# Optimization experiments

Hardware: AMD Instinct MI355X
Metric: run time of the kernel (lower is better)

## Reference

```python
import jax, jax.numpy as jnp
import numpy as np

N, M, DIST, HEADS, D, C, DFFN = 16384, 16, 2, 8, 256, 64, 512
DH = D // HEADS
GRID = 128
BLOCK = 2048  # mirrors torch batch_size loop in find_neighboring_voxels_optimized
EPS = 1e-5


def _neighbors(coords_f, src, m, dist):
    """Blockwise Manhattan-distance topk neighbor gather.
    coords_f: (N,3) float voxel coords; src: (N,D) features.
    Returns (N, m, D) neighbor features, zero-filled where fewer than m in range."""
    n = coords_f.shape[0]
    qblocks = coords_f.reshape(-1, BLOCK, 3)

    def one_block(cb):
        # (BLOCK, N) Manhattan distances
        d = jnp.abs(cb[:, None, :] - coords_f[None, :, :]).sum(-1)
        d = jnp.where(d <= dist, d, jnp.inf)
        vals, idx = jax.lax.top_k(-d, m)          # nearest m (self first: dist 0)
        valid = (vals > -jnp.inf)[..., None]
        return jnp.where(valid, src[idx], jnp.zeros((), src.dtype))

    return jax.lax.map(one_block, qblocks).reshape(n, m, src.shape[-1])


def _layernorm(x, g, b):
    mu = x.mean(-1, keepdims=True)
    var = ((x - mu) ** 2).mean(-1, keepdims=True)
    return (x - mu) * jax.lax.rsqrt(var + EPS) * g + b


def setup_inputs() -> dict:
    key = jax.random.key(0)
    ks = jax.random.split(key, 32)
    p = lambda i, shape, s: jax.random.normal(ks[i], shape, dtype=jnp.float32) * s
    z = lambda shape: jnp.zeros(shape, dtype=jnp.float32)
    o = lambda shape: jnp.ones(shape, dtype=jnp.float32)
    return {
        "coords": jax.random.randint(ks[0], (N, 3), 0, GRID, dtype=jnp.int32),
        "features": jax.random.normal(ks[1], (N, C), dtype=jnp.float32),
        "pe_w1": p(2, (3, D // 2), 0.5), "pe_b1": z((D // 2,)),
        "pe_w2": p(3, (D // 2, D), 0.08), "pe_b2": z((D,)),
        "proj_w": p(4, (C, D), 0.12), "proj_b": z((D,)),
        "wq": p(5, (D, D), 0.06), "bq": z((D,)),
        "wk": p(6, (D, D), 0.06), "bk": z((D,)),
        "wv": p(7, (D, D), 0.06), "bv": z((D,)),
        "wo": p(8, (D, D), 0.06), "bo": z((D,)),
        "ffn_w1": p(9, (D, DFFN), 0.06), "ffn_b1": z((DFFN,)),
        "ffn_w2": p(10, (DFFN, D), 0.04), "ffn_b2": z((D,)),
        "ln_g": o((D,)), "ln_b": z((D,)),
        "fus_w1": p(11, (D, C), 0.06), "fus_b1": z((C,)),
        "fus_w2": p(12, (2 * C, C), 0.09), "fus_b2": z((C,)),
        "bn_g": o((C,)), "bn_b": z((C,)),
    }


def reference(coords, features, pe_w1, pe_b1, pe_w2, pe_b2, proj_w, proj_b,
              wq, bq, wk, bk, wv, bv, wo, bo,
              ffn_w1, ffn_b1, ffn_w2, ffn_b2, ln_g, ln_b,
              fus_w1, fus_b1, fus_w2, fus_b2, bn_g, bn_b):
    coords_f = coords.astype(jnp.float32)
    # dynamic learnable positional encoding on normalized coords
    xn = coords_f / (GRID - 1)
    pe = jax.nn.relu(xn @ pe_w1 + pe_b1) @ pe_w2 + pe_b2
    src = features @ proj_w + proj_b + pe                       # (N, D)

    nf = _neighbors(coords_f, src, M, DIST)                     # (N, M, D)
    query = nf[:, 0, :]                                         # (N, D) self-feature

    # multihead attention: query len 1, key len M, batch N
    q = (query @ wq + bq).reshape(N, HEADS, DH)
    k = (nf @ wk + bk).reshape(N, M, HEADS, DH)
    v = (nf @ wv + bv).reshape(N, M, HEADS, DH)
    scores = jnp.einsum('nhd,nmhd->nhm', q, k) / jnp.sqrt(jnp.float32(DH))
    attn = jax.nn.softmax(scores, axis=-1)
    ao = jnp.einsum('nhm,nmhd->nhd', attn, v).reshape(N, D) @ wo + bo  # (N, D)

    # FFN with residual + LayerNorm (dropout=0 / eval)
    h = jax.nn.relu(ao @ ffn_w1 + ffn_b1) @ ffn_w2 + ffn_b2
    y = _layernorm(ao + h, ln_g, ln_b)                          # (N, D)

    # EnhancedFusion: project, concat, linear, BatchNorm1d (batch stats), ReLU
    t = y @ fus_w1 + fus_b1                                     # (N, C)
    f = jnp.concatenate([features, t], axis=1) @ fus_w2 + fus_b2
    mu = f.mean(0)
    var = ((f - mu) ** 2).mean(0)
    f = (f - mu) * jax.lax.rsqrt(var + EPS) * bn_g + bn_b
    return jax.nn.relu(f)                                       # (N, C)
```

## Files before the change

### kernel.cpp

```cpp
#include <hip/hip_runtime.h>
#include <stdint.h>

typedef unsigned short u16;
typedef unsigned int   u32;
typedef __attribute__((ext_vector_type(8))) short short8;
typedef __attribute__((ext_vector_type(4))) float f32x4;

static constexpr int kN = 16384;
static constexpr float kEPS = 1e-5f;

__device__ __forceinline__ u16 f2bf(float x) {
  u32 u = __float_as_uint(x);
  u32 r = (u + 0x7fffu + ((u >> 16) & 1u)) >> 16;
  return (u16)r;
}
__device__ __forceinline__ float bf2f(u16 x) {
  return __uint_as_float(((u32)x) << 16);
}
__device__ __forceinline__ void ldbf8(const u16* p, float* o) {
  uint4 v = *(const uint4*)p;
  o[0] = __uint_as_float(v.x << 16);  o[1] = __uint_as_float(v.x & 0xffff0000u);
  o[2] = __uint_as_float(v.y << 16);  o[3] = __uint_as_float(v.y & 0xffff0000u);
  o[4] = __uint_as_float(v.z << 16);  o[5] = __uint_as_float(v.z & 0xffff0000u);
  o[6] = __uint_as_float(v.w << 16);  o[7] = __uint_as_float(v.w & 0xffff0000u);
}
__device__ __forceinline__ void gll16(const u16* g, u16* l) {
  __builtin_amdgcn_global_load_lds(
      (const __attribute__((address_space(1))) void*)g,
      (__attribute__((address_space(3))) void*)l, 16, 0, 0);
}

struct WSet {
  const float* s[6]; u16* d[6];
  int K[6]; int N[6]; int dstride[6]; int coff[6];
};

__global__ __launch_bounds__(256) void k_setup(WSet ws,
                                               u32* __restrict__ zero_area,
                                               const float* __restrict__ proj_b,
                                               const float* __restrict__ pe_b2,
                                               const float* __restrict__ uw1,
                                               const float* __restrict__ ub1,
                                               const float* __restrict__ uw2,
                                               const float* __restrict__ ub2,
                                               u16* __restrict__ W2f,
                                               float* __restrict__ bbf,
                                               const int* __restrict__ coords,
                                               const float* __restrict__ feats,
                                               const float* __restrict__ pw1,
                                               const float* __restrict__ pb1,
                                               u16* __restrict__ A1,
                                               u16* __restrict__ A2,
                                               const float* __restrict__ wq,
                                               const float* __restrict__ wk,
                                               const float* __restrict__ wv,
                                               const float* __restrict__ proj_w_f,
                                               const float* __restrict__ pe_w2_f,
                                               u16* __restrict__ W1K,
                                               float* __restrict__ bcomb,
                                               const float* __restrict__ wo_f,
                                               const float* __restrict__ fw1_f,
                                               const float* __restrict__ bo_f,
                                               const float* __restrict__ fb1_f,
                                               u16* __restrict__ woK,
                                               float* __restrict__ bcomb2) {
  int w = blockIdx.y;
  if (w == 6) {
    int idx = blockIdx.x * 256 + threadIdx.x;
    if (idx < 33088) zero_area[idx] = 0u;
    return;
  }
  if (w == 7) {
    int n = blockIdx.x;
    if (n >= 64) return;
    int k = threadIdx.x;
    float s = 0.f;
    for (int j = 0; j < 64; j++) s += uw1[k * 64 + j] * uw2[(64 + j) * 64 + n];
    W2f[n * 320 + k] = f2bf(s);
    if (k < 64) W2f[n * 320 + 256 + k] = f2bf(uw2[k * 64 + n]);
    if (k == 0) {
      float b = ub2[n];
      for (int j = 0; j < 64; j++) b += ub1[j] * uw2[(64 + j) * 64 + n];
      bbf[n] = b;
    }
    return;
  }
  if (w == 8) {
    int r0 = blockIdx.x * 32;
#pragma unroll
    for (int s = 0; s < 3; s++) {
      int j = threadIdx.x + s * 256;
      int row = j / 24, seg = j % 24;
      int n = r0 + row;
      u16 o[8];
      if (seg < 8) {
        const float* fp = feats + (size_t)n * 64 + seg * 8;
        float4 a = *(const float4*)fp;
        float4 b = *(const float4*)(fp + 4);
        o[0] = f2bf(a.x); o[1] = f2bf(a.y); o[2] = f2bf(a.z); o[3] = f2bf(a.w);
        o[4] = f2bf(b.x); o[5] = f2bf(b.y); o[6] = f2bf(b.z); o[7] = f2bf(b.w);
        *(uint4*)(A2 + (size_t)n * 320 + 256 + seg * 8) = *(uint4*)o;
      } else {
        int jj0 = (seg - 8) * 8;
        float x0 = (float)coords[n * 3 + 0] * (1.f / 127.f);
        float x1 = (float)coords[n * 3 + 1] * (1.f / 127.f);
        float x2 = (float)coords[n * 3 + 2] * (1.f / 127.f);
#pragma unroll
        for (int u = 0; u < 8; u++) {
          int jj = jj0 + u;
          float hv = pb1[jj] + x0 * pw1[jj] + x1 * pw1[128 + jj] + x2 * pw1[256 + jj];
          o[u] = f2bf(fmaxf(hv, 0.f));
        }
      }
      *(uint4*)(A1 + (size_t)n * 192 + seg * 8) = *(uint4*)o;
    }
    return;
  }
  if (w == 9) {
    int bx = blockIdx.x;
    if (bx < 3) {
      const float* wsel = (bx == 0) ? wq : (bx == 1) ? wk : wv;
      int c = threadIdx.x;
      float s = 0.f;
      for (int d = 0; d < 256; d++) s += (proj_b[d] + pe_b2[d]) * wsel[d * 256 + c];
      bcomb[bx * 256 + c] = s;
    } else if (bx < 27) {
      int i0 = (bx - 3) * 2048 + threadIdx.x * 8;
      const float* src = (i0 < 16384) ? (proj_w_f + i0) : (pe_w2_f + (i0 - 16384));
      float4 a = *(const float4*)src;
      float4 b = *(const float4*)(src + 4);
      u16 o[8];
      o[0] = f2bf(a.x); o[1] = f2bf(a.y); o[2] = f2bf(a.z); o[3] = f2bf(a.w);
      o[4] = f2bf(b.x); o[5] = f2bf(b.y); o[6] = f2bf(b.z); o[7] = f2bf(b.w);
      *(uint4*)(W1K + i0) = *(uint4*)o;
    } else if (bx < 59) {
      int i0 = (bx - 27) * 2048 + threadIdx.x * 8;
      float4 a = *(const float4*)(wo_f + i0);
      float4 b = *(const float4*)(wo_f + i0 + 4);
      u16 o[8];
      o[0] = f2bf(a.x); o[1] = f2bf(a.y); o[2] = f2bf(a.z); o[3] = f2bf(a.w);
      o[4] = f2bf(b.x); o[5] = f2bf(b.y); o[6] = f2bf(b.z); o[7] = f2bf(b.w);
      *(uint4*)(woK + i0) = *(uint4*)o;
    } else if (bx < 61) {
      int n2 = (bx - 59) * 256 + threadIdx.x;
      float s = fb1_f[n2];
      for (int d = 0; d < 256; d++) s += bo_f[d] * fw1_f[d * 512 + n2];
      bcomb2[n2] = s;
    }
    return;
  }
  const float* S = ws.s[w]; u16* D = ws.d[w];
  int K = ws.K[w], N = ws.N[w], ds = ws.dstride[w], co = ws.coff[w];
  int ntx = N >> 5, tiles = ntx * (K >> 5);
  int t = blockIdx.x;
  if (t >= tiles) return;
  int n0 = (t % ntx) * 32, k0 = (t / ntx) * 32;
  __shared__ float st[32][33];
  int tr = threadIdx.x >> 3, tc4 = (threadIdx.x & 7) * 4;
  float4 v = *(const float4*)(S + (size_t)(k0 + tr) * N + n0 + tc4);
  st[tc4 + 0][tr] = v.x; st[tc4 + 1][tr] = v.y;
  st[tc4 + 2][tr] = v.z; st[tc4 + 3][tr] = v.w;
  __syncthreads();
  u16 o4[4];
  o4[0] = f2bf(st[tr][tc4 + 0]); o4[1] = f2bf(st[tr][tc4 + 1]);
  o4[2] = f2bf(st[tr][tc4 + 2]); o4[3] = f2bf(st[tr][tc4 + 3]);
  *(uint2*)(D + (size_t)(n0 + tr) * ds + co + k0 + tc4) = *(uint2*)o4;
}

__global__ __launch_bounds__(256) void k_combo(const u16* __restrict__ qkvT,
                                               const u16* __restrict__ W1K,
                                               u16* __restrict__ Wcomb,
                                               const u16* __restrict__ fw1T,
                                               const u16* __restrict__ woK,
                                               u16* __restrict__ Wcomb2,
                                               const int* __restrict__ coords,
                                               u32* __restrict__ cnt) {
  int y = blockIdx.y;
  if (y >= 20) {
    int n = ((y - 20) * 4 + blockIdx.x) * 256 + threadIdx.x;
    int c = coords[n * 3] * 128 + coords[n * 3 + 1];
    atomicAdd(&cnt[c], 1u);
    return;
  }
  const u16 *A, *WT; u16* C; int K, N, bm, bn;
  if (y < 12) {
    if (blockIdx.x >= 3) return;
    A = qkvT; WT = W1K; C = Wcomb; K = 256; N = 192;
    bm = y * 64; bn = blockIdx.x * 64;
  } else {
    A = fw1T; WT = woK; C = Wcomb2; K = 256; N = 256;
    bm = (y - 12) * 64; bn = blockIdx.x * 64;
  }
  __shared__ __align__(16) char smem[16384];
  u16* AsB = (u16*)smem;
  u16* BsB = AsB + 2 * 64 * 32;
  u16* tile = (u16*)smem;
  const int tid = threadIdx.x;
  const int wave = tid >> 6, lane = tid & 63;
  const int wr = (wave >> 1) * 32, wc = (wave & 1) * 32;
  const int fr = lane & 15, fk = (lane >> 4) * 8, rq = (lane >> 4) * 4;
  const int grow = tid >> 2, gko = (tid & 3) * 8;

  f32x4 acc[2][2];
#pragma unroll
  for (int i = 0; i < 2; i++)
#pragma unroll
    for (int j = 0; j < 2; j++)
#pragma unroll
      for (int r = 0; r < 4; r++) acc[i][j][r] = 0.f;

  for (int k0 = 0; k0 < K; k0 += 64) {
#pragma unroll
    for (int h = 0; h < 2; h++) {
      gll16(A + (size_t)(bm + grow) * K + k0 + h * 32 + gko, AsB + h * 2048 + tid * 8);
      gll16(WT + (size_t)(bn + grow) * K + k0 + h * 32 + gko, BsB + h * 2048 + tid * 8);
    }
    __syncthreads();
#pragma unroll
    for (int h = 0; h < 2; h++) {
      short8 af[2], bg[2];
#pragma unroll
      for (int i = 0; i < 2; i++)
        af[i] = *(const short8*)&AsB[h * 2048 + (wr + i * 16 + fr) * 32 + fk];
#pragma unroll
      for (int j = 0; j < 2; j++)
        bg[j] = *(const short8*)&BsB[h * 2048 + (wc + j * 16 + fr) * 32 + fk];
#pragma unroll
      for (int i = 0; i < 2; i++)
#pragma unroll
        for (int j = 0; j < 2; j++)
          acc[i][j] = __builtin_amdgcn_mfma_f32_16x16x32_bf16(af[i], bg[j], acc[i][j], 0, 0, 0);
    }
    __syncthreads();
  }
#pragma unroll
  for (int j = 0; j < 2; j++) {
    int ccl = wc + j * 16 + fr;
#pragma unroll
    for (int i = 0; i < 2; i++) {
      int rl = wr + i * 16 + rq;
#pragma unroll
      for (int r = 0; r < 4; r++) tile[(rl + r) * 72 + ccl] = f2bf(acc[i][j][r]);
    }
  }
  __syncthreads();
#pragma unroll
  for (int t = 0; t < 2; t++) {
    int idx = t * 256 + tid;
    int row = idx >> 3, c8 = (idx & 7) * 8;
    *(uint4*)(C + (size_t)(bm + row) * N + bn + c8) = *(const uint4*)&tile[row * 72 + c8];
  }
}

__global__ __launch_bounds__(256) void k_scatter(const int* __restrict__ coords,
                                                 const u32* __restrict__ cnt,
                                                 u32* __restrict__ startb,
                                                 u32* __restrict__ cursor,
                                                 u32* __restrict__ pts) {
  __shared__ u32 sb[16384];
  __shared__ u32 wsum[4];
  int t = threadIdx.x;
  int lane = t & 63, wid = t >> 6;
  int base = t * 64;
  u32 s = 0;
  for (int i = 0; i < 64; i++) s += cnt[base + i];
  u32 v = s;
#pragma unroll
  for (int off = 1; off < 64; off <<= 1) {
    u32 u = __shfl_up(v, off);
    if (lane >= off) v += u;
  }
  if (lane == 63) wsum[wid] = v;
  __syncthreads();
  u32 woff = 0;
  for (int w2 = 0; w2 < wid; w2++) woff += wsum[w2];
  u32 run = woff + v - s;
  for (int i = 0; i < 64; i++) { sb[base + i] = run; run += cnt[base + i]; }
  __syncthreads();
  startb[blockIdx.x * 256 + t] = sb[blockIdx.x * 256 + t];
  int n = blockIdx.x * 256 + t;
  int x = coords[n * 3], y = coords[n * 3 + 1], z = coords[n * 3 + 2];
  int c = x * 128 + y;
  u32 slot = atomicAdd(&cursor[c], 1u);
  pts[sb[c] + slot] = ((u32)z << 14) | (u32)n;
}

template <int BM, int BN, int ACT, bool SEL>
__global__ __launch_bounds__(256) void k_mgemm(
    const u16* __restrict__ A, const u16* __restrict__ WT,
    const float* __restrict__ bias,
    u16* __restrict__ Cout,
    int M, int K, int N, int lda, int ldc,
    const int* __restrict__ coords,
    const u32* __restrict__ startb,
    const u32* __restrict__ cnt,
    const u32* __restrict__ pts,
    int* __restrict__ idxo) {
  if (SEL && (int)blockIdx.y >= M / BM) {
    int sb = ((int)blockIdx.y - M / BM) * gridDim.x + blockIdx.x;
    if (sb >= 64) return;
    int gid = sb * 256 + threadIdx.x;
    u32 pk = pts[gid];
    int n = (int)(pk & 16383u);
    int z = (int)(pk >> 14);
    int x = coords[n * 3], y = coords[n * 3 + 1];
    u32 best[16];
#pragma unroll
    for (int j = 0; j < 16; j++) best[j] = 0xFFFFFFFFu;
    const int dxs[13] = {0, -1, 1, 0, 0, -2, 2, 0, 0, -1, -1, 1, 1};
    const int dys[13] = {0, 0, 0, -1, 1, 0, 0, -2, 2, -1, 1, -1, 1};
    const int dbs[13] = {0, 1, 1, 1, 1, 2, 2, 2, 2, 2, 2, 2, 2};
#pragma unroll
    for (int t = 0; t < 13; t++) {
      int xx = x + dxs[t], yy = y + dys[t];
      if (xx < 0 || xx > 127 || yy < 0 || yy > 127) continue;
      int c = xx * 128 + yy;
      u32 s0 = startb[c], e0 = s0 + cnt[c];
      for (u32 i = s0; i < e0; ++i) {
        u32 p = pts[i];
        int zq = (int)(p >> 14);
        int id = (int)(p & 16383u);
        int az = z - zq; az = az < 0 ? -az : az;
        int dd = dbs[t] + az;
        u32 key = (dd <= 2) ? (((u32)dd << 14) | (u32)id) : 0xFFFFFFFFu;
#pragma unroll
        for (int j = 0; j < 16; j++) {
          u32 lo = min(best[j], key);
          u32 hi = max(best[j], key);
          best[j] = lo; key = hi;
        }
      }
    }
#pragma unroll
    for (int j = 0; j < 16; j++)
      idxo[gid * 16 + j] = (best[j] == 0xFFFFFFFFu) ? -1 : (int)(best[j] & 16383u);
    return;
  }

  constexpr int FM = BM / 32, FN = BN / 32;
  constexpr int RA = BM / 64, RB = BN / 64;
  constexpr int BNP = BN + 8;
  constexpr int STAGE = (BM + BN) * 128;
  constexpr int TILEB = BM * BNP * 2;
  constexpr int SMEMB = STAGE > TILEB ? STAGE : TILEB;
  __shared__ __align__(16) char smem[SMEMB];
  u16* AsB = (u16*)smem;
  u16* BsB = AsB + 2 * BM * 32;
  u16* tile = (u16*)smem;
  const int tid = threadIdx.x;
  const int wave = tid >> 6, lane = tid & 63;
  const int bm = blockIdx.y * BM, bn = blockIdx.x * BN;
  const int wr = (wave >> 1) * (BM / 2), wc = (wave & 1) * (BN / 2);
  const int fr = lane & 15, fk = (lane >> 4) * 8, rq = (lane >> 4) * 4;

  f32x4 acc[FM][FN];
#pragma unroll
  for (int i = 0; i < FM; i++)
#pragma unroll
    for (int j = 0; j < FN; j++)
#pragma unroll
      for (int r = 0; r < 4; r++) acc[i][j][r] = 0.f;

  for (int k0 = 0; k0 < K; k0 += 64) {
#pragma unroll
    for (int h = 0; h < 2; h++) {
#pragma unroll
      for (int r = 0; r < RA; r++) {
        int g2 = r * 256 + tid;
        gll16(A + (size_t)(bm + (g2 >> 2)) * lda + k0 + h * 32 + (g2 & 3) * 8,
              AsB + h * BM * 32 + g2 * 8);
      }
#pragma unroll
      for (int r = 0; r < RB; r++) {
        int g2 = r * 256 + tid;
        gll16(WT + (size_t)(bn + (g2 >> 2)) * K + k0 + h * 32 + (g2 & 3) * 8,
              BsB + h * BN * 32 + g2 * 8);
      }
    }
    __syncthreads();
#pragma unroll
    for (int h = 0; h < 2; h++) {
      short8 af[FM], bg[FN];
#pragma unroll
      for (int i = 0; i < FM; i++)
        af[i] = *(const short8*)&AsB[h * BM * 32 + (wr + i * 16 + fr) * 32 + fk];
#pragma unroll
      for (int j = 0; j < FN; j++)
        bg[j] = *(const short8*)&BsB[h * BN * 32 + (wc + j * 16 + fr) * 32 + fk];
#pragma unroll
      for (int i = 0; i < FM; i++)
#pragma unroll
        for (int j = 0; j < FN; j++)
          acc[i][j] = __builtin_amdgcn_mfma_f32_16x16x32_bf16(af[i], bg[j], acc[i][j], 0, 0, 0);
    }
    __syncthreads();
  }

#pragma unroll
  for (int j = 0; j < FN; j++) {
    int ccl = wc + j * 16 + fr;
    float bval = bias ? bias[bn + ccl] : 0.f;
#pragma unroll
    for (int i = 0; i < FM; i++) {
      int rl = wr + i * 16 + rq;
#pragma unroll
      for (int r = 0; r < 4; r++) {
        float v = acc[i][j][r] + bval;
        if (ACT) v = fmaxf(v, 0.f);
        tile[(rl + r) * BNP + ccl] = f2bf(v);
      }
    }
  }
  __syncthreads();
  constexpr int RPW = BN / 8;
  constexpr int PT = BM * BN / 8 / 256;
#pragma unroll
  for (int t = 0; t < PT; t++) {
    int idx = t * 256 + tid;
    int row = idx / RPW, c8 = (idx % RPW) * 8;
    *(uint4*)(Cout + (size_t)(bm + row) * ldc + bn + c8) =
        *(const uint4*)&tile[row * BNP + c8];
  }
}

__global__ __launch_bounds__(256) void k_attn(const u16* __restrict__ QKV,
                                              const u32* __restrict__ pts,
                                              const int* __restrict__ idx,
                                              const float* __restrict__ bq,
                                              const float* __restrict__ bk,
                                              const float* __restrict__ bv,
                                              u16* __restrict__ outp) {
  int gid = blockIdx.x * 256 + threadIdx.x;
  int s4 = gid >> 3;
  int n = (int)(pts[s4] & 16383u), h = gid & 7;
  const int* ip = idx + s4 * 16;
  const int hb = h * 32;
  float q[32];
  {
    int i0 = ip[0];
    const u16* qp = QKV + (size_t)i0 * 768 + hb;
#pragma unroll
    for (int j = 0; j < 32; j += 8) ldbf8(qp + j, &q[j]);
#pragma unroll
    for (int j = 0; j < 32; j++) q[j] += bq[hb + j];
  }
  float qbk = 0.f;
#pragma unroll
  for (int j = 0; j < 32; j++) qbk += q[j] * bk[hb + j];
  float s[16]; int ii[16];
#pragma unroll
  for (int m = 0; m < 16; m++) {
    int i = ip[m]; ii[m] = i;
    float d = qbk;
    if (i >= 0) {
      const u16* kp = QKV + (size_t)i * 768 + 256 + hb;
      float kv[32];
#pragma unroll
      for (int j = 0; j < 32; j += 8) ldbf8(kp + j, &kv[j]);
#pragma unroll
      for (int j = 0; j < 32; j++) d += q[j] * kv[j];
    }
    s[m] = d * 0.17677669529663689f;
  }
  float mx = s[0];
#pragma unroll
  for (int m = 1; m < 16; m++) mx = fmaxf(mx, s[m]);
  float sum = 0.f;
#pragma unroll
  for (int m = 0; m < 16; m++) { s[m] = __expf(s[m] - mx); sum += s[m]; }
  float inv = 1.f / sum;
  float o[32];
#pragma unroll
  for (int j = 0; j < 32; j++) o[j] = 0.f;
#pragma unroll
  for (int m = 0; m < 16; m++) {
    if (ii[m] >= 0) {
      const u16* vp = QKV + (size_t)ii[m] * 768 + 512 + hb;
      float vv[32];
#pragma unroll
      for (int j = 0; j < 32; j += 8) ldbf8(vp + j, &vv[j]);
#pragma unroll
      for (int j = 0; j < 32; j++) o[j] += s[m] * vv[j];
    }
  }
  u16* op = outp + (size_t)n * 768 + hb;
#pragma unroll
  for (int j = 0; j < 32; j += 8) {
    u16 tmp[8];
#pragma unroll
    for (int jj = 0; jj < 8; jj++) tmp[jj] = f2bf(o[j + jj] * inv + bv[hb + j + jj]);
    *(uint4*)(op + j) = *(uint4*)tmp;
  }
}

__global__ __launch_bounds__(256) void k_ffn2f(const u16* __restrict__ AH,
                                               const u16* __restrict__ WTBIG,
                                               const float* __restrict__ bo,
                                               const float* __restrict__ fb2,
                                               const float* __restrict__ g,
                                               const float* __restrict__ b,
                                               const u16* __restrict__ A2,
                                               const u16* __restrict__ W2f,
                                               const float* __restrict__ bbf,
                                               float* __restrict__ fB,
                                               float* __restrict__ pS,
                                               float* __restrict__ pQ) {
  constexpr int BM = 64, BN = 256, FM = 2, FN = 8;
  constexpr int ADP2 = 328;
  __shared__ __align__(16) char smem[BM * ADP2 * 2];
  __shared__ __align__(16) u16 Bs2[2][2048];
  __shared__ float lnS[64][2], lnQ[64][2];
  __shared__ float colS[64][2], colQ[64][2];
  u16* AsB = (u16*)smem;
  u16* BsB = AsB + 2 * BM * 32;
  u16* aT  = (u16*)smem;
  const int tid = threadIdx.x;
  const int wave = tid >> 6, lane = tid & 63;
  const int bm = blockIdx.x * BM;
  const int wr = (wave >> 1) * 32, wc = (wave & 1) * 128;
  const int fr = lane & 15, fk = (lane >> 4) * 8, rq = (lane >> 4) * 4;

  f32x4 acc[FM][FN];
#pragma unroll
  for (int i = 0; i < FM; i++)
#pragma unroll
    for (int j = 0; j < FN; j++)
#pragma unroll
      for (int r = 0; r < 4; r++) acc[i][j][r] = 0.f;

  for (int k0 = 0; k0 < 768; k0 += 64) {
#pragma unroll
    for (int h = 0; h < 2; h++) {
      {
        int g2 = tid;
        gll16(AH + (size_t)(bm + (g2 >> 2)) * 768 + k0 + h * 32 + (g2 & 3) * 8,
              AsB + h * BM * 32 + g2 * 8);
      }
#pragma unroll
      for (int r = 0; r < 4; r++) {
        int g2 = r * 256 + tid;
        gll16(WTBIG + (size_t)(g2 >> 2) * 768 + k0 + h * 32 + (g2 & 3) * 8,
              BsB + h * BN * 32 + g2 * 8);
      }
    }
    __syncthreads();
#pragma unroll
    for (int h = 0; h < 2; h++) {
      short8 af[FM], bg[FN];
#pragma unroll
      for (int i = 0; i < FM; i++)
        af[i] = *(const short8*)&AsB[h * BM * 32 + (wr + i * 16 + fr) * 32 + fk];
#pragma unroll
      for (int j = 0; j < FN; j++)
        bg[j] = *(const short8*)&BsB[h * BN * 32 + (wc + j * 16 + fr) * 32 + fk];
#pragma unroll
      for (int i = 0; i < FM; i++)
#pragma unroll
        for (int j = 0; j < FN; j++)
          acc[i][j] = __builtin_amdgcn_mfma_f32_16x16x32_bf16(af[i], bg[j], acc[i][j], 0, 0, 0);
    }
    __syncthreads();
  }

#pragma unroll
  for (int j = 0; j < FN; j++) {
    int cc = wc + j * 16 + fr;
    float bval = bo[cc] + fb2[cc];
#pragma unroll
    for (int i = 0; i < FM; i++)
#pragma unroll
      for (int r = 0; r < 4; r++) acc[i][j][r] += bval;
  }
#pragma unroll
  for (int i = 0; i < FM; i++) {
#pragma unroll
    for (int r = 0; r < 4; r++) {
      float sm = 0.f, sq = 0.f;
#pragma unroll
      for (int j = 0; j < FN; j++) { float t = acc[i][j][r]; sm += t; sq += t * t; }
#pragma unroll
      for (int off = 1; off < 16; off <<= 1) {
        sm += __shfl_xor(sm, off);
        sq += __shfl_xor(sq, off);
      }
      if (fr == 0) {
        int row = wr + i * 16 + rq + r;
        lnS[row][wave & 1] = sm;
        lnQ[row][wave & 1] = sq;
      }
    }
  }
  __syncthreads();
#pragma unroll
  for (int i = 0; i < FM; i++) {
#pragma unroll
    for (int r = 0; r < 4; r++) {
      int row = wr + i * 16 + rq + r;
      float sm = lnS[row][0] + lnS[row][1];
      float sq = lnQ[row][0] + lnQ[row][1];
      float mu = sm * (1.f / 256.f);
      float var = sq * (1.f / 256.f) - mu * mu;
      float rstd = rsqrtf(var + kEPS);
#pragma unroll
      for (int j = 0; j < FN; j++) {
        int cc = wc + j * 16 + fr;
        float val = (acc[i][j][r] - mu) * rstd * g[cc] + b[cc];
        aT[row * ADP2 + cc] = f2bf(val);
      }
    }
  }
#pragma unroll
  for (int t = 0; t < 2; t++) {
    int idx = t * 256 + tid;
    int row = idx >> 3, c8 = (idx & 7) * 8;
    *(uint4*)&aT[row * ADP2 + 256 + c8] =
        *(const uint4*)(A2 + (size_t)(bm + row) * 320 + 256 + c8);
  }
  __syncthreads();

  const int wr3 = (wave >> 1) * 32, wc3 = (wave & 1) * 32;
  const int grow = tid >> 2, gko = (tid & 3) * 8;
  f32x4 acc2[2][2];
#pragma unroll
  for (int i = 0; i < 2; i++)
#pragma unroll
    for (int j = 0; j < 2; j++)
#pragma unroll
      for (int r = 0; r < 4; r++) acc2[i][j][r] = 0.f;
  for (int k0 = 0; k0 < 320; k0 += 64) {
#pragma unroll
    for (int h = 0; h < 2; h++)
      gll16(W2f + (size_t)grow * 320 + k0 + h * 32 + gko, Bs2[h] + tid * 8);
    __syncthreads();
#pragma unroll
    for (int h = 0; h < 2; h++) {
      short8 af[2], bg[2];
#pragma unroll
      for (int i = 0; i < 2; i++)
        af[i] = *(const short8*)&aT[(wr3 + i * 16 + fr) * ADP2 + k0 + h * 32 + fk];
#pragma unroll
      for (int j = 0; j < 2; j++)
        bg[j] = *(const short8*)&Bs2[h][(wc3 + j * 16 + fr) * 32 + fk];
#pragma unroll
      for (int i = 0; i < 2; i++)
#pragma unroll
        for (int j = 0; j < 2; j++)
          acc2[i][j] = __builtin_amdgcn_mfma_f32_16x16x32_bf16(af[i], bg[j], acc2[i][j], 0, 0, 0);
    }
    __syncthreads();
  }
  float cS[2] = {0.f, 0.f}, cQ[2] = {0.f, 0.f};
#pragma unroll
  for (int j = 0; j < 2; j++) {
    int col = wc3 + j * 16 + fr;
    float bv = bbf[col];
#pragma unroll
    for (int i = 0; i < 2; i++) {
      int rbase = bm + wr3 + i * 16 + rq;
#pragma unroll
      for (int r = 0; r < 4; r++) {
        float v = acc2[i][j][r] + bv;
        fB[(size_t)(rbase + r) * 64 + col] = v;
        cS[j] += v; cQ[j] += v * v;
      }
    }
  }
#pragma unroll
  for (int off = 16; off < 64; off <<= 1) {
#pragma unroll
    for (int j = 0; j < 2; j++) {
      cS[j] += __shfl_xor(cS[j], off);
      cQ[j] += __shfl_xor(cQ[j], off);
    }
  }
  if ((lane >> 4) == 0) {
#pragma unroll
    for (int j = 0; j < 2; j++) {
      colS[wc3 + j * 16 + fr][wave >> 1] = cS[j];
      colQ[wc3 + j * 16 + fr][wave >> 1] = cQ[j];
    }
  }
  __syncthreads();
  if (tid < 64) {
    atomicAdd(&pS[tid], colS[tid][0] + colS[tid][1]);
    atomicAdd(&pQ[tid], colQ[tid][0] + colQ[tid][1]);
  }
}

__global__ __launch_bounds__(256) void k_bnapply(const float* __restrict__ f,
                                                 const float* __restrict__ pS,
                                                 const float* __restrict__ pQ,
                                                 const float* __restrict__ g,
                                                 const float* __restrict__ b,
                                                 float* __restrict__ out) {
  __shared__ float cf_s[64], sh_s[64];
  if (threadIdx.x < 64) {
    int c = threadIdx.x;
    float S = pS[c], Q = pQ[c];
    float m = S * (1.f / 16384.f);
    float var = Q * (1.f / 16384.f) - m * m;
    float cf = rsqrtf(var + kEPS) * g[c];
    cf_s[c] = cf;
    sh_s[c] = b[c] - m * cf;
  }
  __syncthreads();
  int gid = blockIdx.x * 256 + threadIdx.x;
  int e = gid * 4, col = e & 63;
  float4 v = *(const float4*)(f + e);
  float4 cf = *(const float4*)(cf_s + col);
  float4 sh = *(const float4*)(sh_s + col);
  float4 o;
  o.x = fmaxf(v.x * cf.x + sh.x, 0.f);
  o.y = fmaxf(v.y * cf.y + sh.y, 0.f);
  o.z = fmaxf(v.z * cf.z + sh.z, 0.f);
  o.w = fmaxf(v.w * cf.w + sh.w, 0.f);
  *(float4*)(out + e) = o;
}

extern "C" void kernel_launch(void* const* d_in, const int* in_sizes, int n_in,
                              void* d_out, int out_size, void* d_ws, size_t ws_size,
                              hipStream_t stream) {
  (void)in_sizes; (void)n_in; (void)out_size; (void)ws_size;
  const int*   coords = (const int*)d_in[0];
  const float* feats  = (const float*)d_in[1];
  const float* pe_w1  = (const float*)d_in[2];
  const float* pe_b1  = (const float*)d_in[3];
  const float* pe_w2  = (const float*)d_in[4];
  const float* pe_b2  = (const float*)d_in[5];
  const float* proj_w = (const float*)d_in[6];
  const float* proj_b = (const float*)d_in[7];
  const float* wq  = (const float*)d_in[8];
  const float* bq  = (const float*)d_in[9];
  const float* wk  = (const float*)d_in[10];
  const float* bk  = (const float*)d_in[11];
  const float* wv  = (const float*)d_in[12];
  const float* bv  = (const float*)d_in[13];
  const float* wo  = (const float*)d_in[14];
  const float* bo  = (const float*)d_in[15];
  const float* fw1 = (const float*)d_in[16];
  const float* fb1 = (const float*)d_in[17];
  const float* fw2 = (const float*)d_in[18];
  const float* fb2 = (const float*)d_in[19];
  const float* lng = (const float*)d_in[20];
  const float* lnb = (const float*)d_in[21];
  const float* uw1 = (const float*)d_in[22];
  const float* ub1 = (const float*)d_in[23];
  const float* uw2 = (const float*)d_in[24];
  const float* ub2 = (const float*)d_in[25];
  const float* bng = (const float*)d_in[26];
  const float* bnb = (const float*)d_in[27];
  float* out = (float*)d_out;

  char* Wc = (char*)d_ws;
  const size_t MB = 1u << 20;
  u16*   A1    = (u16*)(Wc + 0 * MB);
  u16*   QKVb  = (u16*)(Wc + 14 * MB);
  u16*   AH    = (u16*)(Wc + 38 * MB);
  u16*   A2    = (u16*)(Wc + 78 * MB);
  float* fB    = (float*)(Wc + 0 * MB);

  u16* qkvT   = (u16*)(Wc + 88 * MB);
  u16* WTBIG  = qkvT + 196608;
  u16* fw1T   = WTBIG + 196608;
  u16* woK    = fw1T + 131072;
  u16* W1K    = woK + 65536;
  u16* W2f    = W1K + 49152;
  u16* Wcomb  = W2f + 20480;
  u16* Wcomb2 = Wcomb + 147456;
  float* bbf    = (float*)(Wcomb2 + 131072);
  float* bcomb  = bbf + 64;
  float* bcomb2 = bcomb + 768;

  u32* Z      = (u32*)(Wc + 90 * MB);
  u32* cnt    = Z;
  u32* cursor = Z + 16384;
  float* pS   = (float*)(Z + 32768);
  float* pQ   = (float*)(Z + 32832);
  u32* startb = Z + 33280;
  u32* pts    = Z + 49664;
  int* idxb   = (int*)(Z + 66048);

  WSet ws;
  ws.s[0] = wq;  ws.d[0] = qkvT;          ws.K[0] = 256; ws.N[0] = 256; ws.dstride[0] = 256; ws.coff[0] = 0;
  ws.s[1] = wk;  ws.d[1] = qkvT + 65536;  ws.K[1] = 256; ws.N[1] = 256; ws.dstride[1] = 256; ws.coff[1] = 0;
  ws.s[2] = wv;  ws.d[2] = qkvT + 131072; ws.K[2] = 256; ws.N[2] = 256; ws.dstride[2] = 256; ws.coff[2] = 0;
  ws.s[3] = wo;  ws.d[3] = WTBIG;         ws.K[3] = 256; ws.N[3] = 256; ws.dstride[3] = 768; ws.coff[3] = 0;
  ws.s[4] = fw1; ws.d[4] = fw1T;          ws.K[4] = 256; ws.N[4] = 512; ws.dstride[4] = 256; ws.coff[4] = 0;
  ws.s[5] = fw2; ws.d[5] = WTBIG;         ws.K[5] = 512; ws.N[5] = 256; ws.dstride[5] = 768; ws.coff[5] = 256;

  k_setup<<<dim3(512, 10), 256, 0, stream>>>(ws, Z, proj_b, pe_b2,
                                             uw1, ub1, uw2, ub2, W2f, bbf,
                                             coords, feats, pe_w1, pe_b1, A1, A2,
                                             wq, wk, wv, proj_w, pe_w2, W1K, bcomb,
                                             wo, fw1, bo, fb1, woK, bcomb2);
  k_combo<<<dim3(4, 36), 256, 0, stream>>>(qkvT, W1K, Wcomb, fw1T, woK, Wcomb2,
                                           coords, cnt);
  k_scatter<<<64, 256, 0, stream>>>(coords, cnt, startb, cursor, pts);
  k_mgemm<128, 128, 0, true><<<dim3(6, 139), 256, 0, stream>>>(
      A1, Wcomb, bcomb, QKVb, kN, 192, 768, 192, 768,
      coords, startb, cnt, pts, idxb);
  k_attn<<<512, 256, 0, stream>>>(QKVb, pts, idxb, bq, bk, bv, AH);
  k_mgemm<128, 128, 1, false><<<dim3(4, 128), 256, 0, stream>>>(
      AH, Wcomb2, bcomb2, AH + 256, kN, 256, 512, 768, 768,
      nullptr, nullptr, nullptr, nullptr, nullptr);
  k_ffn2f<<<256, 256, 0, stream>>>(AH, WTBIG, bo, fb2, lng, lnb,
                                   A2, W2f, bbf, fB, pS, pQ);
  k_bnapply<<<1024, 256, 0, stream>>>(fB, pS, pQ, bng, bnb, out);
}
```

Before: 227.4 us.

## Fuse FFN first-layer GEMM into the FFN-second/LayerNorm/fusion kernel

Removes the separate k_mgemm launch that computed the ReLU hidden activations into a global buffer. k_ffn2f now computes the hidden layer in two 256-wide halves in shared memory and immediately accumulates them against the second FFN weights, so the 512-wide hidden tensor never goes to global memory. The attention output is stored at a compact 256 stride. The cost is more shared memory per block, and only 256 blocks doing more serial work each, which may lower occupancy and parallelism.

```diff
diff --git a/kernel.cpp b/kernel.cpp
--- a/kernel.cpp
+++ b/kernel.cpp
@@ -483,7 +483,7 @@
       for (int j = 0; j < 32; j++) o[j] += s[m] * vv[j];
     }
   }
-  u16* op = outp + (size_t)n * 768 + hb;
+  u16* op = outp + (size_t)n * 256 + hb;
 #pragma unroll
   for (int j = 0; j < 32; j += 8) {
     u16 tmp[8];
@@ -493,8 +493,10 @@
   }
 }
 
-__global__ __launch_bounds__(256) void k_ffn2f(const u16* __restrict__ AH,
+__global__ __launch_bounds__(256) void k_ffn2f(const u16* __restrict__ AO,
                                                const u16* __restrict__ WTBIG,
+                                               const u16* __restrict__ Wcomb2,
+                                               const float* __restrict__ bcomb2,
                                                const float* __restrict__ bo,
                                                const float* __restrict__ fb2,
                                                const float* __restrict__ g,
@@ -505,42 +507,42 @@
                                                float* __restrict__ fB,
                                                float* __restrict__ pS,
                                                float* __restrict__ pQ) {
-  constexpr int BM = 64, BN = 256, FM = 2, FN = 8;
+  constexpr int BM = 64, FM = 2, FN = 8;
   constexpr int ADP2 = 328;
-  __shared__ __align__(16) char smem[BM * ADP2 * 2];
-  __shared__ __align__(16) u16 Bs2[2][2048];
+  constexpr int HDP = 264;
+  __shared__ __align__(16) char smem1[41984];
+  __shared__ __align__(16) char smem2[33792];
   __shared__ float lnS[64][2], lnQ[64][2];
   __shared__ float colS[64][2], colQ[64][2];
-  u16* AsB = (u16*)smem;
-  u16* BsB = AsB + 2 * BM * 32;
-  u16* aT  = (u16*)smem;
+  u16* AsB = (u16*)smem1;
+  u16* BsB = AsB + 2 * 64 * 32;
+  u16* aT  = (u16*)smem1;
+  u16* h1T = (u16*)smem2;
+  u16* Bs2 = (u16*)smem2;
   const int tid = threadIdx.x;
   const int wave = tid >> 6, lane = tid & 63;
   const int bm = blockIdx.x * BM;
   const int wr = (wave >> 1) * 32, wc = (wave & 1) * 128;
   const int fr = lane & 15, fk = (lane >> 4) * 8, rq = (lane >> 4) * 4;
 
-  f32x4 acc[FM][FN];
+  f32x4 xacc[FM][FN];
 #pragma unroll
   for (int i = 0; i < FM; i++)
 #pragma unroll
     for (int j = 0; j < FN; j++)
 #pragma unroll
-      for (int r = 0; r < 4; r++) acc[i][j][r] = 0.f;
-
-  for (int k0 = 0; k0 < 768; k0 += 64) {
+      for (int r = 0; r < 4; r++) xacc[i][j][r] = 0.f;
+
+  for (int k0 = 0; k0 < 256; k0 += 64) {
 #pragma unroll
     for (int h = 0; h < 2; h++) {
-      {
-        int g2 = tid;
-        gll16(AH + (size_t)(bm + (g2 >> 2)) * 768 + k0 + h * 32 + (g2 & 3) * 8,
-              AsB + h * BM * 32 + g2 * 8);
-      }
+      gll16(AO + (size_t)(bm + (tid >> 2)) * 256 + k0 + h * 32 + (tid & 3) * 8,
+            AsB + h * 2048 + tid * 8);
 #pragma unroll
       for (int r = 0; r < 4; r++) {
         int g2 = r * 256 + tid;
         gll16(WTBIG + (size_t)(g2 >> 2) * 768 + k0 + h * 32 + (g2 & 3) * 8,
-              BsB + h * BN * 32 + g2 * 8);
+              BsB + h * 8192 + g2 * 8);
       }
     }
     __syncthreads();
@@ -549,17 +551,101 @@
       short8 af[FM], bg[FN];
 #pragma unroll
       for (int i = 0; i < FM; i++)
-        af[i] = *(const short8*)&AsB[h * BM * 32 + (wr + i * 16 + fr) * 32 + fk];
+        af[i] = *(const short8*)&AsB[h * 2048 + (wr + i * 16 + fr) * 32 + fk];
 #pragma unroll
       for (int j = 0; j < FN; j++)
-        bg[j] = *(const short8*)&BsB[h * BN * 32 + (wc + j * 16 + fr) * 32 + fk];
+        bg[j] = *(const short8*)&BsB[h * 8192 + (wc + j * 16 + fr) * 32 + fk];
 #pragma unroll
       for (int i = 0; i < FM; i++)
 #pragma unroll
         for (int j = 0; j < FN; j++)
-          acc[i][j] = __builtin_amdgcn_mfma_f32_16x16x32_bf16(af[i], bg[j], acc[i][j], 0, 0, 0);
+          xacc[i][j] = __builtin_amdgcn_mfma_f32_16x16x32_bf16(af[i], bg[j], xacc[i][j], 0, 0, 0);
     }
     __syncthreads();
+  }
+
+#pragma unroll
+  for (int half = 0; half < 2; half++) {
+    f32x4 hacc[FM][FN];
+#pragma unroll
+    for (int i = 0; i < FM; i++)
+#pragma unroll
+      for (int j = 0; j < FN; j++)
+#pragma unroll
+        for (int r = 0; r < 4; r++) hacc[i][j][r] = 0.f;
+    const u16* Wc2 = Wcomb2 + (size_t)half * 256 * 256;
+    for (int k0 = 0; k0 < 256; k0 += 64) {
+#pragma unroll
+      for (int h = 0; h < 2; h++) {
+        gll16(AO + (size_t)(bm + (tid >> 2)) * 256 + k0 + h * 32 + (tid & 3) * 8,
+              AsB + h * 2048 + tid * 8);
+#pragma unroll
+        for (int r = 0; r < 4; r++) {
+          int g2 = r * 256 + tid;
+          gll16(Wc2 + (size_t)(g2 >> 2) * 256 + k0 + h * 32 + (g2 & 3) * 8,
+                BsB + h * 8192 + g2 * 8);
+        }
+      }
+      __syncthreads();
+#pragma unroll
+      for (int h = 0; h < 2; h++) {
+        short8 af[FM], bg[FN];
+#pragma unroll
+        for (int i = 0; i < FM; i++)
+          af[i] = *(const short8*)&AsB[h * 2048 + (wr + i * 16 + fr) * 32 + fk];
+#pragma unroll
+        for (int j = 0; j < FN; j++)
+          bg[j] = *(const short8*)&BsB[h * 8192 + (wc + j * 16 + fr) * 32 + fk];
+#pragma unroll
+        for (int i = 0; i < FM; i++)
+#pragma unroll
+          for (int j = 0; j < FN; j++)
+            hacc[i][j] = __builtin_amdgcn_mfma_f32_16x16x32_bf16(af[i], bg[j], hacc[i][j], 0, 0, 0);
+      }
+      __syncthreads();
+    }
+#pragma unroll
+    for (int j = 0; j < FN; j++) {
+      int cc = wc + j * 16 + fr;
+      float bval = bcomb2[half * 256 + cc];
+#pragma unroll
+      for (int i = 0; i < FM; i++) {
+        int rl = wr + i * 16 + rq;
+#pragma unroll
+        for (int r = 0; r < 4; r++)
+          h1T[(rl + r) * HDP + cc] = f2bf(fmaxf(hacc[i][j][r] + bval, 0.f));
+      }
+    }
+    __syncthreads();
+    const int kbase = 256 + half * 256;
+    for (int k0 = 0; k0 < 256; k0 += 64) {
+#pragma unroll
+      for (int h = 0; h < 2; h++) {
+#pragma unroll
+        for (int r = 0; r < 4; r++) {
+          int g2 = r * 256 + tid;
+          gll16(WTBIG + (size_t)(g2 >> 2) * 768 + kbase + k0 + h * 32 + (g2 & 3) * 8,
+                BsB + h * 8192 + g2 * 8);
+        }
+      }
+      __syncthreads();
+#pragma unroll
+      for (int h = 0; h < 2; h++) {
+        short8 af[FM], bg[FN];
+#pragma unroll
+        for (int i = 0; i < FM; i++)
+          af[i] = *(const short8*)&h1T[(wr + i * 16 + fr) * HDP + k0 + h * 32 + fk];
+#pragma unroll
+        for (int j = 0; j < FN; j++)
+          bg[j] = *(const short8*)&BsB[h * 8192 + (wc + j * 16 + fr) * 32 + fk];
+#pragma unroll
+        for (int i = 0; i < FM; i++)
+#pragma unroll
+          for (int j = 0; j < FN; j++)
+            xacc[i][j] = __builtin_amdgcn_mfma_f32_16x16x32_bf16(af[i], bg[j], xacc[i][j], 0, 0, 0);
+      }
+      __syncthreads();
+    }
   }
 
 #pragma unroll
@@ -569,7 +655,7 @@
 #pragma unroll
     for (int i = 0; i < FM; i++)
 #pragma unroll
-      for (int r = 0; r < 4; r++) acc[i][j][r] += bval;
+      for (int r = 0; r < 4; r++) xacc[i][j][r] += bval;
   }
 #pragma unroll
   for (int i = 0; i < FM; i++) {
@@ -577,7 +663,7 @@
     for (int r = 0; r < 4; r++) {
       float sm = 0.f, sq = 0.f;
 #pragma unroll
-      for (int j = 0; j < FN; j++) { float t = acc[i][j][r]; sm += t; sq += t * t; }
+      for (int j = 0; j < FN; j++) { float t = xacc[i][j][r]; sm += t; sq += t * t; }
 #pragma unroll
       for (int off = 1; off < 16; off <<= 1) {
         sm += __shfl_xor(sm, off);
@@ -604,7 +690,7 @@
 #pragma unroll
       for (int j = 0; j < FN; j++) {
         int cc = wc + j * 16 + fr;
-        float val = (acc[i][j][r] - mu) * rstd * g[cc] + b[cc];
+        float val = (xacc[i][j][r] - mu) * rstd * g[cc] + b[cc];
         aT[row * ADP2 + cc] = f2bf(val);
       }
     }
@@ -630,7 +716,7 @@
   for (int k0 = 0; k0 < 320; k0 += 64) {
 #pragma unroll
     for (int h = 0; h < 2; h++)
-      gll16(W2f + (size_t)grow * 320 + k0 + h * 32 + gko, Bs2[h] + tid * 8);
+      gll16(W2f + (size_t)grow * 320 + k0 + h * 32 + gko, Bs2 + h * 2048 + tid * 8);
     __syncthreads();
 #pragma unroll
     for (int h = 0; h < 2; h++) {
@@ -640,7 +726,7 @@
         af[i] = *(const short8*)&aT[(wr3 + i * 16 + fr) * ADP2 + k0 + h * 32 + fk];
 #pragma unroll
       for (int j = 0; j < 2; j++)
-        bg[j] = *(const short8*)&Bs2[h][(wc3 + j * 16 + fr) * 32 + fk];
+        bg[j] = *(const short8*)&Bs2[h * 2048 + (wc3 + j * 16 + fr) * 32 + fk];
 #pragma unroll
       for (int i = 0; i < 2; i++)
 #pragma unroll
@@ -755,7 +841,7 @@
   const size_t MB = 1u << 20;
   u16*   A1    = (u16*)(Wc + 0 * MB);
   u16*   QKVb  = (u16*)(Wc + 14 * MB);
-  u16*   AH    = (u16*)(Wc + 38 * MB);
+  u16*   AO    = (u16*)(Wc + 38 * MB);
   u16*   A2    = (u16*)(Wc + 78 * MB);
   float* fB    = (float*)(Wc + 0 * MB);
 
@@ -799,11 +885,8 @@
   k_mgemm<128, 128, 0, true><<<dim3(6, 139), 256, 0, stream>>>(
       A1, Wcomb, bcomb, QKVb, kN, 192, 768, 192, 768,
       coords, startb, cnt, pts, idxb);
-  k_attn<<<512, 256, 0, stream>>>(QKVb, pts, idxb, bq, bk, bv, AH);
-  k_mgemm<128, 128, 1, false><<<dim3(4, 128), 256, 0, stream>>>(
-      AH, Wcomb2, bcomb2, AH + 256, kN, 256, 512, 768, 768,
-      nullptr, nullptr, nullptr, nullptr, nullptr);
-  k_ffn2f<<<256, 256, 0, stream>>>(AH, WTBIG, bo, fb2, lng, lnb,
+  k_attn<<<512, 256, 0, stream>>>(QKVb, pts, idxb, bq, bk, bv, AO);
+  k_ffn2f<<<256, 256, 0, stream>>>(AO, WTBIG, Wcomb2, bcomb2, bo, fb2, lng, lnb,
                                    A2, W2f, bbf, fB, pS, pQ);
   k_bnapply<<<1024, 256, 0, stream>>>(fB, pS, pQ, bng, bnb, out);
 }
```

Result: slower. 235.8 us (+3.7%).
